# Kernel optimization log

Hardware: AMD Instinct MI355X
Metric: run time of the kernel (lower is better)

## Reference

```python
import jax, jax.numpy as jnp
import numpy as np

# snntorch default ATan surrogate (alpha=2): fwd = heaviside, bwd = g / (1 + (pi*x)^2)
@jax.custom_vjp
def atan_spike(x):
    return (x > 0).astype(x.dtype)

def _atan_fwd(x):
    return atan_spike(x), x

def _atan_bwd(x, g):
    return (g / (1.0 + (jnp.pi * x) ** 2),)

atan_spike.defvjp(_atan_fwd, _atan_bwd)

B = 4096  # batch
D = 100   # row length / fc1 in-features; also number of timesteps (rows)
O = 3     # fc1 out-features

def setup_inputs() -> dict:
    key = jax.random.key(0)
    k1, k2, k3, k4 = jax.random.split(key, 4)
    x = jax.random.uniform(k1, (B, D, D), jnp.float32)   # rate-coding probabilities
    u = jax.random.uniform(k2, (B, D, D), jnp.float32)   # Bernoulli uniforms for rate coding
    lim = 1.0 / np.sqrt(D)
    W = jax.random.uniform(k3, (O, D), jnp.float32, -lim, lim)
    b = jax.random.uniform(k4, (O,), jnp.float32, -lim, lim)
    beta = jnp.float32(0.95)
    threshold = jnp.float32(1.0)
    return {"x": x, "u": u, "W": W, "b": b, "beta": beta, "threshold": threshold}

def reference(x, u, W, b, beta, threshold):
    # sgen.rate(x, 1)[0]: one-step Bernoulli rate coding, prob = x
    spikes = (u < x).astype(x.dtype)            # [B, 100, 100]
    seq = jnp.transpose(spikes, (1, 0, 2))      # [T=100, B, 100] (loop over rows)

    def step(mem, inp):                          # mem: [B, 3], inp: [B, 100]
        cur = inp @ W.T + b                      # fc1
        # snntorch Leaky, reset_mechanism='subtract': reset from previous mem, detached
        reset = jax.lax.stop_gradient(atan_spike(mem - threshold))
        mem = beta * mem + cur - reset * threshold
        spk = atan_spike(mem - threshold)
        return mem, (spk, mem)

    mem0 = jnp.zeros((x.shape[0], O), x.dtype)   # init_leaky()
    _, (spk_rec, mem_rec) = jax.lax.scan(step, mem0, seq)
    return spk_rec, mem_rec                      # each [100, B, 3]
```

## Files before the change

kernel.cpp:

```cpp
#include <hip/hip_runtime.h>

#define NB 4096
#define ND 100
#define NT 100
#define NO 3
#define PITCH 101

__global__ __launch_bounds__(384) void cur_kernel(
    const float* __restrict__ x, const float* __restrict__ u,
    const float* __restrict__ W, const float* __restrict__ bias,
    float* __restrict__ cur_out)
{
    __shared__ float sp[NT * PITCH];
    __shared__ float Ws[NO * PITCH];
    __shared__ float bs[NO];

    const int b   = blockIdx.x;
    const int tid = threadIdx.x;

    if (tid < NO * ND) {
        int o = tid / ND;
        int d = tid - o * ND;
        Ws[o * PITCH + d] = W[tid];
    }
    if (tid < NO) bs[tid] = bias[tid];

    const float4* x4 = (const float4*)(x + (size_t)b * (ND * ND));
    const float4* u4 = (const float4*)(u + (size_t)b * (ND * ND));
    for (int i = tid; i < (ND * ND) / 4; i += 384) {
        float4 xv = x4[i];
        float4 uv = u4[i];
        int f   = i * 4;
        int row = f / ND;
        int col = f - row * ND;
        float* p = &sp[row * PITCH + col];
        p[0] = (uv.x < xv.x) ? 1.0f : 0.0f;
        p[1] = (uv.y < xv.y) ? 1.0f : 0.0f;
        p[2] = (uv.z < xv.z) ? 1.0f : 0.0f;
        p[3] = (uv.w < xv.w) ? 1.0f : 0.0f;
    }
    __syncthreads();

    if (tid < NO * NT) {
        int o = tid / NT;
        int t = tid - o * NT;
        const float* sr = &sp[t * PITCH];
        const float* wr = &Ws[o * PITCH];
        float acc = bs[o];
#pragma unroll 10
        for (int d = 0; d < ND; ++d)
            acc = fmaf(sr[d], wr[d], acc);
        cur_out[(size_t)b * (NT * NO) + t * NO + o] = acc;
    }
}

__global__ __launch_bounds__(64) void scan_kernel(
    const float* __restrict__ cur,
    const float* __restrict__ beta_p, const float* __restrict__ thr_p,
    float* __restrict__ out)
{
    const int tid = blockIdx.x * 64 + threadIdx.x;
    const int b = tid / NO;
    const int o = tid - b * NO;
    const float beta = beta_p[0];
    const float thr  = thr_p[0];

    const float* c = cur + (size_t)b * (NT * NO) + o;
    float* mem_rec = out + (size_t)NT * NB * NO;

    float mem = 0.0f;
#pragma unroll 5
    for (int t = 0; t < NT; ++t) {
        float cv = c[t * NO];
        float rsub = (mem > thr) ? thr : 0.0f;
        mem = __fadd_rn(__fadd_rn(__fmul_rn(beta, mem), cv), -rsub);
        float s = (mem > thr) ? 1.0f : 0.0f;
        out[(size_t)t * (NB * NO) + tid]      = s;
        mem_rec[(size_t)t * (NB * NO) + tid]  = mem;
    }
}

extern "C" void kernel_launch(void* const* d_in, const int* in_sizes, int n_in,
                              void* d_out, int out_size, void* d_ws, size_t ws_size,
                              hipStream_t stream) {
    const float* x    = (const float*)d_in[0];
    const float* u    = (const float*)d_in[1];
    const float* W    = (const float*)d_in[2];
    const float* bias = (const float*)d_in[3];
    const float* beta = (const float*)d_in[4];
    const float* thr  = (const float*)d_in[5];
    float* out = (float*)d_out;

    float* cur_ws = (float*)d_ws;

    cur_kernel<<<NB, 384, 0, stream>>>(x, u, W, bias, cur_ws);
    scan_kernel<<<(NB * NO) / 64, 64, 0, stream>>>(cur_ws, beta, thr, out);
}
```

Before: 351.0 us.

## Fuse rate-coding matvec and LIF scan into one kernel, per-row threads

Merges the current-computation kernel and the membrane scan kernel into one launch that keeps the per-timestep currents in shared memory rather than a global workspace. Each thread now reads one full row of x and u with float4 loads and accumulates all three outputs directly, with no spike matrix staged in LDS. The scan runs on only 6 threads per block and writes outputs with a stride of 12 bytes, so the stores are poorly coalesced and serialized behind the compute. Per-thread row reads are also strided by 400 bytes across lanes, which coalesces worse than the old contiguous loads.

```diff
diff --git a/kernel.cpp b/kernel.cpp
--- a/kernel.cpp
+++ b/kernel.cpp
@@ -4,79 +4,74 @@
 #define ND 100
 #define NT 100
 #define NO 3
-#define PITCH 101
+#define BPB 2
+#define THREADS 256
+#define NROW (BPB * NT)
 
-__global__ __launch_bounds__(384) void cur_kernel(
+__global__ __launch_bounds__(THREADS) void fused_kernel(
     const float* __restrict__ x, const float* __restrict__ u,
     const float* __restrict__ W, const float* __restrict__ bias,
-    float* __restrict__ cur_out)
+    const float* __restrict__ beta_p, const float* __restrict__ thr_p,
+    float* __restrict__ out)
 {
-    __shared__ float sp[NT * PITCH];
-    __shared__ float Ws[NO * PITCH];
-    __shared__ float bs[NO];
+    __shared__ float4 W4[NO][ND / 4];
+    __shared__ float  bs[NO];
+    __shared__ float  curS[BPB][NT][NO];
 
-    const int b   = blockIdx.x;
     const int tid = threadIdx.x;
+    const int b0  = blockIdx.x * BPB;
 
-    if (tid < NO * ND) {
-        int o = tid / ND;
-        int d = tid - o * ND;
-        Ws[o * PITCH + d] = W[tid];
+    if (tid < NO * (ND / 4)) {
+        W4[tid / (ND / 4)][tid % (ND / 4)] = ((const float4*)W)[tid];
     }
     if (tid < NO) bs[tid] = bias[tid];
+    __syncthreads();
 
-    const float4* x4 = (const float4*)(x + (size_t)b * (ND * ND));
-    const float4* u4 = (const float4*)(u + (size_t)b * (ND * ND));
-    for (int i = tid; i < (ND * ND) / 4; i += 384) {
-        float4 xv = x4[i];
-        float4 uv = u4[i];
-        int f   = i * 4;
-        int row = f / ND;
-        int col = f - row * ND;
-        float* p = &sp[row * PITCH + col];
-        p[0] = (uv.x < xv.x) ? 1.0f : 0.0f;
-        p[1] = (uv.y < xv.y) ? 1.0f : 0.0f;
-        p[2] = (uv.z < xv.z) ? 1.0f : 0.0f;
-        p[3] = (uv.w < xv.w) ? 1.0f : 0.0f;
+    if (tid < NROW) {
+        const int lb = tid / NT;
+        const int t  = tid - lb * NT;
+        const size_t R = (size_t)(b0 + lb) * NT + t;
+        const float4* xr = (const float4*)(x + R * ND);
+        const float4* ur = (const float4*)(u + R * ND);
+        float a0 = bs[0], a1 = bs[1], a2 = bs[2];
+#pragma unroll
+        for (int i = 0; i < ND / 4; ++i) {
+            float4 xv = xr[i];
+            float4 uv = ur[i];
+            float4 w0 = W4[0][i];
+            float4 w1 = W4[1][i];
+            float4 w2 = W4[2][i];
+            float s;
+            s = (uv.x < xv.x) ? 1.0f : 0.0f;
+            a0 = fmaf(s, w0.x, a0); a1 = fmaf(s, w1.x, a1); a2 = fmaf(s, w2.x, a2);
+            s = (uv.y < xv.y) ? 1.0f : 0.0f;
+            a0 = fmaf(s, w0.y, a0); a1 = fmaf(s, w1.y, a1); a2 = fmaf(s, w2.y, a2);
+            s = (uv.z < xv.z) ? 1.0f : 0.0f;
+            a0 = fmaf(s, w0.z, a0); a1 = fmaf(s, w1.z, a1); a2 = fmaf(s, w2.z, a2);
+            s = (uv.w < xv.w) ? 1.0f : 0.0f;
+            a0 = fmaf(s, w0.w, a0); a1 = fmaf(s, w1.w, a1); a2 = fmaf(s, w2.w, a2);
+        }
+        curS[lb][t][0] = a0;
+        curS[lb][t][1] = a1;
+        curS[lb][t][2] = a2;
     }
     __syncthreads();
 
-    if (tid < NO * NT) {
-        int o = tid / NT;
-        int t = tid - o * NT;
-        const float* sr = &sp[t * PITCH];
-        const float* wr = &Ws[o * PITCH];
-        float acc = bs[o];
-#pragma unroll 10
-        for (int d = 0; d < ND; ++d)
-            acc = fmaf(sr[d], wr[d], acc);
-        cur_out[(size_t)b * (NT * NO) + t * NO + o] = acc;
-    }
-}
-
-__global__ __launch_bounds__(64) void scan_kernel(
-    const float* __restrict__ cur,
-    const float* __restrict__ beta_p, const float* __restrict__ thr_p,
-    float* __restrict__ out)
-{
-    const int tid = blockIdx.x * 64 + threadIdx.x;
-    const int b = tid / NO;
-    const int o = tid - b * NO;
-    const float beta = beta_p[0];
-    const float thr  = thr_p[0];
-
-    const float* c = cur + (size_t)b * (NT * NO) + o;
-    float* mem_rec = out + (size_t)NT * NB * NO;
-
-    float mem = 0.0f;
-#pragma unroll 5
-    for (int t = 0; t < NT; ++t) {
-        float cv = c[t * NO];
-        float rsub = (mem > thr) ? thr : 0.0f;
-        mem = __fadd_rn(__fadd_rn(__fmul_rn(beta, mem), cv), -rsub);
-        float s = (mem > thr) ? 1.0f : 0.0f;
-        out[(size_t)t * (NB * NO) + tid]      = s;
-        mem_rec[(size_t)t * (NB * NO) + tid]  = mem;
+    if (tid < BPB * NO) {
+        const int lb = tid / NO;
+        const int o  = tid - lb * NO;
+        const int bo = (b0 + lb) * NO + o;
+        const float beta = beta_p[0];
+        const float thr  = thr_p[0];
+        float* mem_rec = out + (size_t)NT * NB * NO;
+        float mem = 0.0f;
+        for (int t = 0; t < NT; ++t) {
+            float cv = curS[lb][t][o];
+            float rsub = (mem > thr) ? thr : 0.0f;
+            mem = __fadd_rn(__fadd_rn(__fmul_rn(beta, mem), cv), -rsub);
+            out[(size_t)t * (NB * NO) + bo]     = (mem > thr) ? 1.0f : 0.0f;
+            mem_rec[(size_t)t * (NB * NO) + bo] = mem;
+        }
     }
 }
 
@@ -91,8 +86,5 @@
     const float* thr  = (const float*)d_in[5];
     float* out = (float*)d_out;
 
-    float* cur_ws = (float*)d_ws;
-
-    cur_kernel<<<NB, 384, 0, stream>>>(x, u, W, bias, cur_ws);
-    scan_kernel<<<(NB * NO) / 64, 64, 0, stream>>>(cur_ws, beta, thr, out);
+    fused_kernel<<<NB / BPB, THREADS, 0, stream>>>(x, u, W, bias, beta, thr, out);
 }
```

Result: slower. 425.1 us (+21.1%).

## Fuse current computation and membrane scan into one kernel with byte-packed spikes

Applied to the files above, without the earlier changes.

Merges the fc1 current kernel and the leaky scan kernel into a single launch. Currents now stay in shared memory, so the global workspace round trip and the second launch go away. Spikes are packed four per 32-bit word in shared memory, which cuts LDS footprint, and the block shrinks to 256 threads for higher occupancy. In exchange, only 3 threads per block run the 100-step serial scan, and their output stores are scattered (stride 3 within a block), which may leave the tail of each block poorly utilised.

```diff
diff --git a/kernel.cpp b/kernel.cpp
--- a/kernel.cpp
+++ b/kernel.cpp
@@ -4,79 +4,74 @@
 #define ND 100
 #define NT 100
 #define NO 3
-#define PITCH 101
+#define THREADS 256
+#define SPW 27
 
-__global__ __launch_bounds__(384) void cur_kernel(
+__global__ __launch_bounds__(THREADS, 8) void fused_kernel(
     const float* __restrict__ x, const float* __restrict__ u,
     const float* __restrict__ W, const float* __restrict__ bias,
-    float* __restrict__ cur_out)
+    const float* __restrict__ beta_p, const float* __restrict__ thr_p,
+    float* __restrict__ out)
 {
-    __shared__ float sp[NT * PITCH];
-    __shared__ float Ws[NO * PITCH];
+    __shared__ unsigned int sp[NT * SPW];
+    __shared__ float Ws[NO * ND];
     __shared__ float bs[NO];
+    __shared__ float curS[NT * 4];
 
+    const int tid = threadIdx.x;
     const int b   = blockIdx.x;
-    const int tid = threadIdx.x;
 
-    if (tid < NO * ND) {
-        int o = tid / ND;
-        int d = tid - o * ND;
-        Ws[o * PITCH + d] = W[tid];
-    }
+    if (tid < (NO * ND) / 4) ((float4*)Ws)[tid] = ((const float4*)W)[tid];
     if (tid < NO) bs[tid] = bias[tid];
 
     const float4* x4 = (const float4*)(x + (size_t)b * (ND * ND));
     const float4* u4 = (const float4*)(u + (size_t)b * (ND * ND));
-    for (int i = tid; i < (ND * ND) / 4; i += 384) {
+    for (int i = tid; i < (ND * ND) / 4; i += THREADS) {
         float4 xv = x4[i];
         float4 uv = u4[i];
-        int f   = i * 4;
-        int row = f / ND;
-        int col = f - row * ND;
-        float* p = &sp[row * PITCH + col];
-        p[0] = (uv.x < xv.x) ? 1.0f : 0.0f;
-        p[1] = (uv.y < xv.y) ? 1.0f : 0.0f;
-        p[2] = (uv.z < xv.z) ? 1.0f : 0.0f;
-        p[3] = (uv.w < xv.w) ? 1.0f : 0.0f;
+        int row = i / (ND / 4);
+        int c4  = i - row * (ND / 4);
+        unsigned int p = (uv.x < xv.x ? 1u        : 0u)
+                       | (uv.y < xv.y ? 0x100u    : 0u)
+                       | (uv.z < xv.z ? 0x10000u  : 0u)
+                       | (uv.w < xv.w ? 0x1000000u: 0u);
+        sp[row * SPW + c4] = p;
     }
     __syncthreads();
 
-    if (tid < NO * NT) {
-        int o = tid / NT;
-        int t = tid - o * NT;
-        const float* sr = &sp[t * PITCH];
-        const float* wr = &Ws[o * PITCH];
+    for (int task = tid; task < NO * NT; task += THREADS) {
+        int o = task / NT;
+        int t = task - o * NT;
+        const unsigned int* sr = &sp[t * SPW];
+        const float*        wr = &Ws[o * ND];
         float acc = bs[o];
-#pragma unroll 10
-        for (int d = 0; d < ND; ++d)
-            acc = fmaf(sr[d], wr[d], acc);
-        cur_out[(size_t)b * (NT * NO) + t * NO + o] = acc;
+#pragma unroll 5
+        for (int j = 0; j < ND / 4; ++j) {
+            unsigned int m = sr[j];
+            acc = fmaf((float)( m        & 0xffu), wr[4 * j + 0], acc);
+            acc = fmaf((float)((m >> 8 ) & 0xffu), wr[4 * j + 1], acc);
+            acc = fmaf((float)((m >> 16) & 0xffu), wr[4 * j + 2], acc);
+            acc = fmaf((float)( m >> 24        ), wr[4 * j + 3], acc);
+        }
+        curS[t * 4 + o] = acc;
     }
-}
+    __syncthreads();
 
-__global__ __launch_bounds__(64) void scan_kernel(
-    const float* __restrict__ cur,
-    const float* __restrict__ beta_p, const float* __restrict__ thr_p,
-    float* __restrict__ out)
-{
-    const int tid = blockIdx.x * 64 + threadIdx.x;
-    const int b = tid / NO;
-    const int o = tid - b * NO;
-    const float beta = beta_p[0];
-    const float thr  = thr_p[0];
-
-    const float* c = cur + (size_t)b * (NT * NO) + o;
-    float* mem_rec = out + (size_t)NT * NB * NO;
-
-    float mem = 0.0f;
-#pragma unroll 5
-    for (int t = 0; t < NT; ++t) {
-        float cv = c[t * NO];
-        float rsub = (mem > thr) ? thr : 0.0f;
-        mem = __fadd_rn(__fadd_rn(__fmul_rn(beta, mem), cv), -rsub);
-        float s = (mem > thr) ? 1.0f : 0.0f;
-        out[(size_t)t * (NB * NO) + tid]      = s;
-        mem_rec[(size_t)t * (NB * NO) + tid]  = mem;
+    if (tid < NO) {
+        const int o  = tid;
+        const int bo = b * NO + o;
+        const float beta = beta_p[0];
+        const float thr  = thr_p[0];
+        float* mem_rec = out + (size_t)NT * NB * NO;
+        float mem = 0.0f;
+#pragma unroll 4
+        for (int t = 0; t < NT; ++t) {
+            float cv = curS[t * 4 + o];
+            float rsub = (mem > thr) ? thr : 0.0f;
+            mem = __fadd_rn(__fadd_rn(__fmul_rn(beta, mem), cv), -rsub);
+            out[(size_t)t * (NB * NO) + bo]     = (mem > thr) ? 1.0f : 0.0f;
+            mem_rec[(size_t)t * (NB * NO) + bo] = mem;
+        }
     }
 }
 
@@ -91,8 +86,5 @@
     const float* thr  = (const float*)d_in[5];
     float* out = (float*)d_out;
 
-    float* cur_ws = (float*)d_ws;
-
-    cur_kernel<<<NB, 384, 0, stream>>>(x, u, W, bias, cur_ws);
-    scan_kernel<<<(NB * NO) / 64, 64, 0, stream>>>(cur_ws, beta, thr, out);
+    fused_kernel<<<NB, THREADS, 0, stream>>>(x, u, W, bias, beta, thr, out);
 }
```

Measured after the change: 357.5 us. Within noise of the previous version (+1.9%).
